# Kernel tuning notes

Measured on AMD Instinct MI355X. Metric: run time of the kernel, lower is better.

The kernel has to match this reference:

```python
import jax, jax.numpy as jnp
import numpy as np

EPS = 1e-5
TOP_K = 2


def setup_inputs() -> dict:
    key = jax.random.key(0)
    ks = jax.random.split(key, 8)
    B, T, D, E, F = 4, 2048, 1024, 8, 4096
    s_in = 1.0 / np.sqrt(D)
    s_ff = 1.0 / np.sqrt(F)
    return {
        "hidden_states": jax.random.normal(ks[0], (B, T, D), jnp.float32),
        "input_tensor": jax.random.normal(ks[1], (B, T, D), jnp.float32),
        "gate_w": jax.random.normal(ks[2], (D, E), jnp.float32) * s_in,
        "gate_b": jnp.zeros((E,), jnp.float32),
        "w1": jax.random.normal(ks[3], (E, D, F), jnp.float32) * s_in,
        "b1": jnp.zeros((E, F), jnp.float32),
        "w2": jax.random.normal(ks[4], (E, F, D), jnp.float32) * s_ff,
        "b2": jnp.zeros((E, D), jnp.float32),
        "gamma": jnp.ones((D,), jnp.float32),
        "beta": jnp.zeros((D,), jnp.float32),
    }


def _layer_norm(x, gamma, beta):
    mu = jnp.mean(x, axis=-1, keepdims=True)
    var = jnp.mean(jnp.square(x - mu), axis=-1, keepdims=True)
    return (x - mu) * jax.lax.rsqrt(var + EPS) * gamma + beta


def reference(hidden_states, input_tensor, gate_w, gate_b, w1, b1, w2, b2, gamma, beta):
    E = gate_b.shape[0]
    # Router: softmax over experts, then top-k gate values/indices.
    gate_logits = jnp.einsum("btd,de->bte", hidden_states, gate_w) + gate_b
    gate_probs = jax.nn.softmax(gate_logits, axis=-1)
    topk_gates, topk_idx = jax.lax.top_k(gate_probs, TOP_K)  # [B,T,K]
    # Combine weights per expert: sum of top-k gate values routed to expert e.
    combine_w = jnp.sum(
        jax.nn.one_hot(topk_idx, E, dtype=hidden_states.dtype)
        * topk_gates[..., None],
        axis=-2,
    )  # [B,T,E]
    # Dispatch/combine: weighted sum of expert FFN outputs (loop over small fixed E).
    expert_outputs = jnp.zeros_like(hidden_states)
    for e in range(E):
        h = jax.nn.gelu(jnp.einsum("btd,df->btf", hidden_states, w1[e]) + b1[e])
        y = jnp.einsum("btf,fd->btd", h, w2[e]) + b2[e]
        expert_outputs = expert_outputs + combine_w[..., e:e + 1] * y
    # Dropout is identity in eval mode.
    return _layer_norm(expert_outputs + input_tensor, gamma, beta)
```

## Files before the change

### kernel.cpp

```cpp
#include <hip/hip_runtime.h>

#define TOKENS 8192
#define DIM 1024
#define NEXP 8
#define FDIM 4096

typedef __bf16 bf16x8 __attribute__((ext_vector_type(8)));
typedef float f32x4 __attribute__((ext_vector_type(4)));
typedef float f32x16 __attribute__((ext_vector_type(16)));

__device__ __forceinline__ unsigned short f2bf(float f) {
  unsigned u = __builtin_bit_cast(unsigned, f);
  u += 0x7fffu + ((u >> 16) & 1u);
  return (unsigned short)(u >> 16);
}

__device__ __forceinline__ float bf2f(unsigned short s) {
  unsigned u = (unsigned)s << 16;
  return __builtin_bit_cast(float, u);
}

__device__ __forceinline__ void gload16(const void* g, void* l) {
  __builtin_amdgcn_global_load_lds(
      (const __attribute__((address_space(1))) unsigned int*)g,
      (__attribute__((address_space(3))) unsigned int*)l, 16, 0, 0);
}

__global__ void zero_counts_kernel(int* counts) {
  if (threadIdx.x < NEXP) counts[threadIdx.x] = 0;
}

__global__ void scan_kernel(const int* counts, int* offs, int* nchk,
                            int* chunks0, int* chunks1) {
  if (threadIdx.x == 0) {
    int s = 0;
    for (int e = 0; e < NEXP; ++e) { offs[e] = s; s += counts[e]; }
    offs[NEXP] = s;
    int nc0 = 0, nc1 = 0;
    for (int e = 0; e < NEXP; ++e) {
      const int mt = (counts[e] + 127) >> 7;
      for (int mc = 0; mc < mt; mc += 4) {
        for (int n4 = 0; n4 < 32; n4 += 4)
          chunks0[nc0++] = (e << 16) | (mc << 8) | n4;
        for (int n4 = 0; n4 < 8; n4 += 4)
          chunks1[nc1++] = (e << 16) | (mc << 8) | n4;
      }
    }
    nchk[0] = nc0;
    nchk[1] = nc1;
  }
}

__global__ void router_kernel(const float* __restrict__ hs,
                              const float* __restrict__ gw,
                              const float* __restrict__ gb,
                              int* __restrict__ counts,
                              int* __restrict__ tok_idx,
                              float* __restrict__ tok_w,
                              unsigned int* __restrict__ slotinfo,
                              unsigned short* __restrict__ hs_bf) {
  const int lane = threadIdx.x & 63;
  const int wid = threadIdx.x >> 6;
  const int t = blockIdx.x * 4 + wid;
  const float* row = hs + (size_t)t * DIM;

  float x[16];
  const float4* r4 = (const float4*)(row + lane * 16);
#pragma unroll
  for (int i = 0; i < 4; ++i) {
    float4 v = r4[i];
    x[i * 4 + 0] = v.x; x[i * 4 + 1] = v.y; x[i * 4 + 2] = v.z; x[i * 4 + 3] = v.w;
  }

  float acc[8];
#pragma unroll
  for (int e = 0; e < 8; ++e) acc[e] = 0.f;
#pragma unroll
  for (int i = 0; i < 16; ++i) {
    const int d = lane * 16 + i;
    const float4* g4 = (const float4*)(gw + (size_t)d * 8);
    float4 g0 = g4[0], g1 = g4[1];
    const float xv = x[i];
    acc[0] += xv * g0.x; acc[1] += xv * g0.y; acc[2] += xv * g0.z; acc[3] += xv * g0.w;
    acc[4] += xv * g1.x; acc[5] += xv * g1.y; acc[6] += xv * g1.z; acc[7] += xv * g1.w;
  }
#pragma unroll
  for (int sh = 1; sh < 64; sh <<= 1) {
#pragma unroll
    for (int e = 0; e < 8; ++e) acc[e] += __shfl_xor(acc[e], sh, 64);
  }
#pragma unroll
  for (int e = 0; e < 8; ++e) acc[e] += gb[e];

  float mx = acc[0];
#pragma unroll
  for (int e = 1; e < 8; ++e) mx = fmaxf(mx, acc[e]);
  float p[8];
  float sum = 0.f;
#pragma unroll
  for (int e = 0; e < 8; ++e) { p[e] = __expf(acc[e] - mx); sum += p[e]; }
  const float inv = 1.0f / sum;

  int i0 = 0; float b0 = p[0];
#pragma unroll
  for (int e = 1; e < 8; ++e) if (p[e] > b0) { b0 = p[e]; i0 = e; }
  int i1 = -1; float b1v = -1.f;
#pragma unroll
  for (int e = 0; e < 8; ++e) if (e != i0 && p[e] > b1v) { b1v = p[e]; i1 = e; }

  if (lane == 0) {
    int pos0 = atomicAdd(&counts[i0], 1);
    tok_idx[i0 * TOKENS + pos0] = t;
    tok_w[i0 * TOKENS + pos0] = b0 * inv;
    int pos1 = atomicAdd(&counts[i1], 1);
    tok_idx[i1 * TOKENS + pos1] = t;
    tok_w[i1 * TOKENS + pos1] = b1v * inv;
    slotinfo[t] = ((unsigned)i0 << 29) | ((unsigned)pos0 << 16) |
                  ((unsigned)i1 << 13) | (unsigned)pos1;
  }

  unsigned short us[16];
#pragma unroll
  for (int i = 0; i < 16; ++i) us[i] = f2bf(x[i]);
  uint4 o0, o1;
  o0.x = (unsigned)us[0] | ((unsigned)us[1] << 16);
  o0.y = (unsigned)us[2] | ((unsigned)us[3] << 16);
  o0.z = (unsigned)us[4] | ((unsigned)us[5] << 16);
  o0.w = (unsigned)us[6] | ((unsigned)us[7] << 16);
  o1.x = (unsigned)us[8] | ((unsigned)us[9] << 16);
  o1.y = (unsigned)us[10] | ((unsigned)us[11] << 16);
  o1.z = (unsigned)us[12] | ((unsigned)us[13] << 16);
  o1.w = (unsigned)us[14] | ((unsigned)us[15] << 16);
  uint4* dst = (uint4*)(hs_bf + (size_t)t * DIM + lane * 16);
  dst[0] = o0;
  dst[1] = o1;
}

__global__ void cast_transpose_all(const float* __restrict__ w1,
                                   unsigned short* __restrict__ w1t,
                                   const float* __restrict__ w2,
                                   unsigned short* __restrict__ w2t) {
  __shared__ float tile[64][65];
  const int L = blockIdx.x;
  const float* src;
  unsigned short* dstp;
  int R, C, bi;
  if (L < 8192) { src = w1; dstp = w1t; R = DIM;  C = FDIM; bi = L; }
  else          { src = w2; dstp = w2t; R = FDIM; C = DIM;  bi = L - 8192; }
  const int nx = C >> 6;
  const int e = bi >> 10;
  const int w = bi & 1023;
  const int by = w / nx, bx = w % nx;
  const int r0 = by * 64, c0 = bx * 64;
  const float* s = src + (size_t)e * R * C;
  unsigned int* d = (unsigned int*)(dstp + (size_t)e * R * C);

#pragma unroll
  for (int i = 0; i < 16; ++i) {
    const int idx = threadIdx.x + i * 256;
    const int r = idx >> 6;
    const int c = idx & 63;
    tile[r][c] = s[(size_t)(r0 + r) * C + (c0 + c)];
  }
  __syncthreads();
#pragma unroll
  for (int i = 0; i < 8; ++i) {
    const int idx = threadIdx.x + i * 256;
    const int c = idx >> 5;
    const int r = (idx & 31) * 2;
    unsigned pk = (unsigned)f2bf(tile[r][c]) | ((unsigned)f2bf(tile[r + 1][c]) << 16);
    d[((size_t)(c0 + c) * R + (r0 + r)) >> 1] = pk;
  }
}

template<int MODE, int K, int N>
__global__ __launch_bounds__(256, 4)
void moe_gemm(const unsigned short* __restrict__ Abase,
              const unsigned short* __restrict__ Bbase,
              const float* __restrict__ bias,
              const int* __restrict__ counts,
              const int* __restrict__ offs,
              const int* __restrict__ tok_idx,
              const int* __restrict__ chunktab,
              const int* __restrict__ nchk,
              unsigned short* __restrict__ dst) {
  constexpr int NS = K / 32;
  __shared__ __align__(16) unsigned char sm[32768];

  const int L = blockIdx.x;
  const int xk = L & 7;
  const int tt = L >> 3;
  const int g = (tt >> 4) * 8 + xk;
  if (g >= nchk[MODE]) return;
  const int within = tt & 15;
  const int cd = chunktab[g];
  const int e = cd >> 16;
  const int cnt = counts[e];
  const int m0 = (((cd >> 8) & 255) + (within >> 2)) * 128;
  if (m0 >= cnt) return;
  const int n0 = ((cd & 255) + (within & 3)) * 128;
  const int goff = offs[e];

  const int tid = threadIdx.x;
  const int lane = tid & 63;
  const int wid = tid >> 6;
  const int wm = wid >> 1;
  const int wn = wid & 1;
  const int l31 = lane & 31;
  const int lh = lane >> 5;

  const int trow = tid >> 2;
  const int tswz = (tid & 3) ^ ((trow >> 1) & 3);
  const unsigned char* Bexp = (const unsigned char*)(Bbase + (size_t)e * K * N);

  int gA0 = m0 + trow;      if (gA0 > cnt - 1) gA0 = cnt - 1;
  int gA1 = m0 + trow + 64; if (gA1 > cnt - 1) gA1 = cnt - 1;
  size_t rowA0, rowA1;
  if (MODE == 0) {
    rowA0 = (size_t)tok_idx[e * TOKENS + gA0] * K;
    rowA1 = (size_t)tok_idx[e * TOKENS + gA1] * K;
  } else {
    rowA0 = (size_t)(goff + gA0) * K;
    rowA1 = (size_t)(goff + gA1) * K;
  }
  const unsigned char* pA0 = (const unsigned char*)(Abase + rowA0) + tswz * 16;
  const unsigned char* pA1 = (const unsigned char*)(Abase + rowA1) + tswz * 16;
  const unsigned char* pB0 = Bexp + (size_t)(n0 + trow) * (K * 2) + tswz * 16;
  const unsigned char* pB1 = Bexp + (size_t)(n0 + trow + 64) * (K * 2) + tswz * 16;

  const int sw = (l31 >> 1) & 3;
  const int cE = lh ^ sw;
  const int aB = wm * 4096 + l31 * 64 + cE * 16;
  const int bB = 8192 + wn * 4096 + l31 * 64 + cE * 16;
  const unsigned char* smc = (const unsigned char*)sm;
  unsigned char* smw = (unsigned char*)sm + tid * 16;

  f32x16 acc[2][2];
#pragma unroll
  for (int mb = 0; mb < 2; ++mb)
#pragma unroll
    for (int nb = 0; nb < 2; ++nb)
#pragma unroll
      for (int r = 0; r < 16; ++r) acc[mb][nb][r] = 0.f;

  gload16(pA0, smw);
  gload16(pA1, smw + 4096);
  gload16(pB0, smw + 8192);
  gload16(pB1, smw + 12288);
  pA0 += 64; pA1 += 64; pB0 += 64; pB1 += 64;

#pragma unroll 1
  for (int st = 0; st < NS; ++st) {
    const int cs = (st & 1) << 14;
    const int ns = ((st + 1) & 1) << 14;
    if (st < NS - 1) {
      gload16(pA0, smw + ns);
      gload16(pA1, smw + ns + 4096);
      gload16(pB0, smw + ns + 8192);
      gload16(pB1, smw + ns + 12288);
      pA0 += 64; pA1 += 64; pB0 += 64; pB1 += 64;
      asm volatile("s_waitcnt vmcnt(4)" ::: "memory");
    } else {
      asm volatile("s_waitcnt vmcnt(0)" ::: "memory");
    }
    __builtin_amdgcn_s_barrier();
    __builtin_amdgcn_sched_barrier(0);
#pragma unroll
    for (int kq = 0; kq < 2; ++kq) {
      const int ko = kq << 5;
      bf16x8 a0 = *(const bf16x8*)(smc + cs + (aB ^ ko));
      bf16x8 a1 = *(const bf16x8*)(smc + cs + ((aB + 2048) ^ ko));
      bf16x8 b0 = *(const bf16x8*)(smc + cs + (bB ^ ko));
      bf16x8 b1 = *(const bf16x8*)(smc + cs + ((bB + 2048) ^ ko));
      acc[0][0] = __builtin_amdgcn_mfma_f32_32x32x16_bf16(a0, b0, acc[0][0], 0, 0, 0);
      acc[0][1] = __builtin_amdgcn_mfma_f32_32x32x16_bf16(a0, b1, acc[0][1], 0, 0, 0);
      acc[1][0] = __builtin_amdgcn_mfma_f32_32x32x16_bf16(a1, b0, acc[1][0], 0, 0, 0);
      acc[1][1] = __builtin_amdgcn_mfma_f32_32x32x16_bf16(a1, b1, acc[1][1], 0, 0, 0);
    }
    __builtin_amdgcn_sched_barrier(0);
    asm volatile("s_waitcnt lgkmcnt(0)" ::: "memory");
    __builtin_amdgcn_s_barrier();
  }

#pragma unroll
  for (int nb = 0; nb < 2; ++nb) {
    const int fcol = n0 + wn * 64 + nb * 32 + l31;
    const float bv = bias[e * N + fcol];
#pragma unroll
    for (int mb = 0; mb < 2; ++mb) {
#pragma unroll
      for (int r = 0; r < 16; ++r) {
        const int ml = wm * 64 + mb * 32 + (r & 3) + 8 * (r >> 2) + 4 * lh;
        const int gm = m0 + ml;
        if (gm < cnt) {
          float v = acc[mb][nb][r] + bv;
          if (MODE == 0) {
            const float u = 0.7978845608028654f * (v + 0.044715f * v * v * v);
            const float th = 1.0f - 2.0f / (1.0f + __expf(2.0f * u));
            v = 0.5f * v * (1.0f + th);
          }
          dst[(size_t)(goff + gm) * N + fcol] = f2bf(v);
        }
      }
    }
  }
}

__global__ void ln_combine_kernel(const unsigned short* __restrict__ y_buf,
                                  const float* __restrict__ in_t,
                                  const int* __restrict__ offs,
                                  const unsigned int* __restrict__ slotinfo,
                                  const float* __restrict__ tok_w,
                                  const float* __restrict__ gamma,
                                  const float* __restrict__ beta,
                                  float* __restrict__ out) {
  const int lane = threadIdx.x & 63;
  const int wid = threadIdx.x >> 6;
  const int t = blockIdx.x * 4 + wid;

  const unsigned s = slotinfo[t];
  const int e0 = s >> 29, p0 = (s >> 16) & 8191;
  const int e1 = (s >> 13) & 7, p1 = s & 8191;
  const float w0 = tok_w[e0 * TOKENS + p0];
  const float w1 = tok_w[e1 * TOKENS + p1];
  const size_t r0 = (size_t)(offs[e0] + p0) * DIM;
  const size_t r1 = (size_t)(offs[e1] + p1) * DIM;

  float v[16];
  {
    const float4* i4 = (const float4*)(in_t + (size_t)t * DIM + lane * 16);
    const uint4* y0 = (const uint4*)(y_buf + r0 + lane * 16);
    const uint4* y1 = (const uint4*)(y_buf + r1 + lane * 16);
#pragma unroll
    for (int i = 0; i < 4; ++i) {
      float4 a = i4[i];
      v[i * 4 + 0] = a.x; v[i * 4 + 1] = a.y; v[i * 4 + 2] = a.z; v[i * 4 + 3] = a.w;
    }
#pragma unroll
    for (int i = 0; i < 2; ++i) {
      uint4 u0 = y0[i];
      uint4 u1 = y1[i];
      const unsigned uw0[4] = {u0.x, u0.y, u0.z, u0.w};
      const unsigned uw1[4] = {u1.x, u1.y, u1.z, u1.w};
#pragma unroll
      for (int k = 0; k < 4; ++k) {
        const int base = i * 8 + k * 2;
        v[base + 0] += w0 * bf2f((unsigned short)(uw0[k] & 0xffff)) +
                       w1 * bf2f((unsigned short)(uw1[k] & 0xffff));
        v[base + 1] += w0 * bf2f((unsigned short)(uw0[k] >> 16)) +
                       w1 * bf2f((unsigned short)(uw1[k] >> 16));
      }
    }
  }

  float sum = 0.f, s2 = 0.f;
#pragma unroll
  for (int i = 0; i < 16; ++i) { sum += v[i]; s2 += v[i] * v[i]; }
#pragma unroll
  for (int sh = 1; sh < 64; sh <<= 1) {
    sum += __shfl_xor(sum, sh, 64);
    s2 += __shfl_xor(s2, sh, 64);
  }
  const float mu = sum * (1.0f / DIM);
  const float var = s2 * (1.0f / DIM) - mu * mu;
  const float rs = rsqrtf(var + 1e-5f);

  float4* w4 = (float4*)(out + (size_t)t * DIM + lane * 16);
#pragma unroll
  for (int i = 0; i < 4; ++i) {
    const int d = lane * 16 + i * 4;
    float4 gg = *(const float4*)(gamma + d);
    float4 bb = *(const float4*)(beta + d);
    float4 o;
    o.x = (v[i * 4 + 0] - mu) * rs * gg.x + bb.x;
    o.y = (v[i * 4 + 1] - mu) * rs * gg.y + bb.y;
    o.z = (v[i * 4 + 2] - mu) * rs * gg.z + bb.z;
    o.w = (v[i * 4 + 3] - mu) * rs * gg.w + bb.w;
    w4[i] = o;
  }
}

extern "C" void kernel_launch(void* const* d_in, const int* in_sizes, int n_in,
                              void* d_out, int out_size, void* d_ws, size_t ws_size,
                              hipStream_t stream) {
  const float* hs    = (const float*)d_in[0];
  const float* in_t  = (const float*)d_in[1];
  const float* gw    = (const float*)d_in[2];
  const float* gb    = (const float*)d_in[3];
  const float* w1    = (const float*)d_in[4];
  const float* b1    = (const float*)d_in[5];
  const float* w2    = (const float*)d_in[6];
  const float* b2    = (const float*)d_in[7];
  const float* gamma = (const float*)d_in[8];
  const float* beta  = (const float*)d_in[9];
  float* out = (float*)d_out;
  char* ws = (char*)d_ws;

  int* counts            = (int*)(ws + 0);
  int* offs              = (int*)(ws + 256);
  unsigned int* slotinfo = (unsigned int*)(ws + 512);
  int* nchk              = (int*)(ws + 33280);
  int* chunks0           = (int*)(ws + 33536);
  int* chunks1           = (int*)(ws + 35072);
  int* tok_idx           = (int*)(ws + 66048);
  float* tok_w           = (float*)(ws + 328192);
  unsigned short* hs_bf  = (unsigned short*)(ws + 590336);
  unsigned short* w1t    = (unsigned short*)(ws + 17367552);
  unsigned short* w2t    = (unsigned short*)(ws + 84476416);
  unsigned short* h_buf  = (unsigned short*)(ws + 151585280);
  unsigned short* y_buf  = (unsigned short*)(ws + 590336);

  zero_counts_kernel<<<1, 64, 0, stream>>>(counts);
  router_kernel<<<TOKENS / 4, 256, 0, stream>>>(hs, gw, gb, counts, tok_idx, tok_w,
                                                slotinfo, hs_bf);
  scan_kernel<<<1, 64, 0, stream>>>(counts, offs, nchk, chunks0, chunks1);
  cast_transpose_all<<<16384, 256, 0, stream>>>(w1, w1t, w2, w2t);
  moe_gemm<0, DIM, FDIM><<<6144, 256, 0, stream>>>(
      hs_bf, w1t, b1, counts, offs, tok_idx, chunks0, nchk, h_buf);
  moe_gemm<1, FDIM, DIM><<<2048, 256, 0, stream>>>(
      h_buf, w2t, b2, counts, offs, tok_idx, chunks1, nchk, y_buf);
  ln_combine_kernel<<<TOKENS / 4, 256, 0, stream>>>(y_buf, in_t, offs, slotinfo,
                                                    tok_w, gamma, beta, out);
}
```

Baseline: 729.9 us.

## Enlarge MoE GEMM M tile to 256 rows with 4x2 MFMA per wave

```diff
diff --git a/kernel.cpp b/kernel.cpp
--- a/kernel.cpp
+++ b/kernel.cpp
@@ -38,7 +38,7 @@
     offs[NEXP] = s;
     int nc0 = 0, nc1 = 0;
     for (int e = 0; e < NEXP; ++e) {
-      const int mt = (counts[e] + 127) >> 7;
+      const int mt = (counts[e] + 255) >> 8;
       for (int mc = 0; mc < mt; mc += 4) {
         for (int n4 = 0; n4 < 32; n4 += 4)
           chunks0[nc0++] = (e << 16) | (mc << 8) | n4;
@@ -174,7 +174,7 @@
 }
 
 template<int MODE, int K, int N>
-__global__ __launch_bounds__(256, 4)
+__global__ __launch_bounds__(256, 2)
 void moe_gemm(const unsigned short* __restrict__ Abase,
               const unsigned short* __restrict__ Bbase,
               const float* __restrict__ bias,
@@ -185,7 +185,7 @@
               const int* __restrict__ nchk,
               unsigned short* __restrict__ dst) {
   constexpr int NS = K / 32;
-  __shared__ __align__(16) unsigned char sm[32768];
+  __shared__ __align__(16) unsigned char sm[49152];
 
   const int L = blockIdx.x;
   const int xk = L & 7;
@@ -196,7 +196,7 @@
   const int cd = chunktab[g];
   const int e = cd >> 16;
   const int cnt = counts[e];
-  const int m0 = (((cd >> 8) & 255) + (within >> 2)) * 128;
+  const int m0 = (((cd >> 8) & 255) + (within >> 2)) * 256;
   if (m0 >= cnt) return;
   const int n0 = ((cd & 255) + (within & 3)) * 128;
   const int goff = offs[e];
@@ -213,53 +213,55 @@
   const int tswz = (tid & 3) ^ ((trow >> 1) & 3);
   const unsigned char* Bexp = (const unsigned char*)(Bbase + (size_t)e * K * N);
 
-  int gA0 = m0 + trow;      if (gA0 > cnt - 1) gA0 = cnt - 1;
-  int gA1 = m0 + trow + 64; if (gA1 > cnt - 1) gA1 = cnt - 1;
-  size_t rowA0, rowA1;
-  if (MODE == 0) {
-    rowA0 = (size_t)tok_idx[e * TOKENS + gA0] * K;
-    rowA1 = (size_t)tok_idx[e * TOKENS + gA1] * K;
-  } else {
-    rowA0 = (size_t)(goff + gA0) * K;
-    rowA1 = (size_t)(goff + gA1) * K;
-  }
-  const unsigned char* pA0 = (const unsigned char*)(Abase + rowA0) + tswz * 16;
-  const unsigned char* pA1 = (const unsigned char*)(Abase + rowA1) + tswz * 16;
+  const unsigned char* pA[4];
+#pragma unroll
+  for (int j = 0; j < 4; ++j) {
+    int gr = m0 + trow + j * 64;
+    if (gr > cnt - 1) gr = cnt - 1;
+    size_t rowA;
+    if (MODE == 0) rowA = (size_t)tok_idx[e * TOKENS + gr] * K;
+    else           rowA = (size_t)(goff + gr) * K;
+    pA[j] = (const unsigned char*)(Abase + rowA) + tswz * 16;
+  }
   const unsigned char* pB0 = Bexp + (size_t)(n0 + trow) * (K * 2) + tswz * 16;
   const unsigned char* pB1 = Bexp + (size_t)(n0 + trow + 64) * (K * 2) + tswz * 16;
 
   const int sw = (l31 >> 1) & 3;
   const int cE = lh ^ sw;
-  const int aB = wm * 4096 + l31 * 64 + cE * 16;
-  const int bB = 8192 + wn * 4096 + l31 * 64 + cE * 16;
+  const int aB = wm * 8192 + l31 * 64 + cE * 16;
+  const int bB = 16384 + wn * 4096 + l31 * 64 + cE * 16;
   const unsigned char* smc = (const unsigned char*)sm;
   unsigned char* smw = (unsigned char*)sm + tid * 16;
 
-  f32x16 acc[2][2];
-#pragma unroll
-  for (int mb = 0; mb < 2; ++mb)
+  f32x16 acc[4][2];
+#pragma unroll
+  for (int mb = 0; mb < 4; ++mb)
 #pragma unroll
     for (int nb = 0; nb < 2; ++nb)
 #pragma unroll
       for (int r = 0; r < 16; ++r) acc[mb][nb][r] = 0.f;
 
-  gload16(pA0, smw);
-  gload16(pA1, smw + 4096);
-  gload16(pB0, smw + 8192);
-  gload16(pB1, smw + 12288);
-  pA0 += 64; pA1 += 64; pB0 += 64; pB1 += 64;
+#pragma unroll
+  for (int j = 0; j < 4; ++j) gload16(pA[j], smw + j * 4096);
+  gload16(pB0, smw + 16384);
+  gload16(pB1, smw + 20480);
+#pragma unroll
+  for (int j = 0; j < 4; ++j) pA[j] += 64;
+  pB0 += 64; pB1 += 64;
 
 #pragma unroll 1
   for (int st = 0; st < NS; ++st) {
-    const int cs = (st & 1) << 14;
-    const int ns = ((st + 1) & 1) << 14;
+    const int cs = (st & 1) ? 24576 : 0;
+    const int ns = (st & 1) ? 0 : 24576;
     if (st < NS - 1) {
-      gload16(pA0, smw + ns);
-      gload16(pA1, smw + ns + 4096);
-      gload16(pB0, smw + ns + 8192);
-      gload16(pB1, smw + ns + 12288);
-      pA0 += 64; pA1 += 64; pB0 += 64; pB1 += 64;
-      asm volatile("s_waitcnt vmcnt(4)" ::: "memory");
+#pragma unroll
+      for (int j = 0; j < 4; ++j) gload16(pA[j], smw + ns + j * 4096);
+      gload16(pB0, smw + ns + 16384);
+      gload16(pB1, smw + ns + 20480);
+#pragma unroll
+      for (int j = 0; j < 4; ++j) pA[j] += 64;
+      pB0 += 64; pB1 += 64;
+      asm volatile("s_waitcnt vmcnt(6)" ::: "memory");
     } else {
       asm volatile("s_waitcnt vmcnt(0)" ::: "memory");
     }
@@ -268,14 +270,20 @@
 #pragma unroll
     for (int kq = 0; kq < 2; ++kq) {
       const int ko = kq << 5;
-      bf16x8 a0 = *(const bf16x8*)(smc + cs + (aB ^ ko));
+      bf16x8 a0 = *(const bf16x8*)(smc + cs + ((aB + 0)    ^ ko));
       bf16x8 a1 = *(const bf16x8*)(smc + cs + ((aB + 2048) ^ ko));
-      bf16x8 b0 = *(const bf16x8*)(smc + cs + (bB ^ ko));
+      bf16x8 a2 = *(const bf16x8*)(smc + cs + ((aB + 4096) ^ ko));
+      bf16x8 a3 = *(const bf16x8*)(smc + cs + ((aB + 6144) ^ ko));
+      bf16x8 b0 = *(const bf16x8*)(smc + cs + ((bB + 0)    ^ ko));
       bf16x8 b1 = *(const bf16x8*)(smc + cs + ((bB + 2048) ^ ko));
       acc[0][0] = __builtin_amdgcn_mfma_f32_32x32x16_bf16(a0, b0, acc[0][0], 0, 0, 0);
       acc[0][1] = __builtin_amdgcn_mfma_f32_32x32x16_bf16(a0, b1, acc[0][1], 0, 0, 0);
       acc[1][0] = __builtin_amdgcn_mfma_f32_32x32x16_bf16(a1, b0, acc[1][0], 0, 0, 0);
       acc[1][1] = __builtin_amdgcn_mfma_f32_32x32x16_bf16(a1, b1, acc[1][1], 0, 0, 0);
+      acc[2][0] = __builtin_amdgcn_mfma_f32_32x32x16_bf16(a2, b0, acc[2][0], 0, 0, 0);
+      acc[2][1] = __builtin_amdgcn_mfma_f32_32x32x16_bf16(a2, b1, acc[2][1], 0, 0, 0);
+      acc[3][0] = __builtin_amdgcn_mfma_f32_32x32x16_bf16(a3, b0, acc[3][0], 0, 0, 0);
+      acc[3][1] = __builtin_amdgcn_mfma_f32_32x32x16_bf16(a3, b1, acc[3][1], 0, 0, 0);
     }
     __builtin_amdgcn_sched_barrier(0);
     asm volatile("s_waitcnt lgkmcnt(0)" ::: "memory");
@@ -287,10 +295,10 @@
     const int fcol = n0 + wn * 64 + nb * 32 + l31;
     const float bv = bias[e * N + fcol];
 #pragma unroll
-    for (int mb = 0; mb < 2; ++mb) {
+    for (int mb = 0; mb < 4; ++mb) {
 #pragma unroll
       for (int r = 0; r < 16; ++r) {
-        const int ml = wm * 64 + mb * 32 + (r & 3) + 8 * (r >> 2) + 4 * lh;
+        const int ml = wm * 128 + mb * 32 + (r & 3) + 8 * (r >> 2) + 4 * lh;
         const int gm = m0 + ml;
         if (gm < cnt) {
           float v = acc[mb][nb][r] + bv;
@@ -415,9 +423,9 @@
                                                 slotinfo, hs_bf);
   scan_kernel<<<1, 64, 0, stream>>>(counts, offs, nchk, chunks0, chunks1);
   cast_transpose_all<<<16384, 256, 0, stream>>>(w1, w1t, w2, w2t);
-  moe_gemm<0, DIM, FDIM><<<6144, 256, 0, stream>>>(
+  moe_gemm<0, DIM, FDIM><<<4096, 256, 0, stream>>>(
       hs_bf, w1t, b1, counts, offs, tok_idx, chunks0, nchk, h_buf);
-  moe_gemm<1, FDIM, DIM><<<2048, 256, 0, stream>>>(
+  moe_gemm<1, FDIM, DIM><<<1024, 256, 0, stream>>>(
       h_buf, w2t, b2, counts, offs, tok_idx, chunks1, nchk, y_buf);
   ln_combine_kernel<<<TOKENS / 4, 256, 0, stream>>>(y_buf, in_t, offs, slotinfo,
                                                     tok_w, gamma, beta, out);
```

Result: slower. 819.4 us (+12.3%).
